# Performance work log

Hardware: AMD Instinct MI355X
Metric: run time of the kernel (lower is better)

Reference implementation:

```python
import jax, jax.numpy as jnp
import numpy as np
from jax.scipy.special import logsumexp

D = 256            # descriptor_dim == output_dim
H = 4              # attention heads (hard-coded in AttentionalGNN)
DH = D // H        # 64 per-head dim
KNN = 20           # k for dynamic kNN graph
N_LAYERS = 18      # ['self','cross'] * 9
SINKHORN_ITERS = 20
MATCH_THRESHOLD = 0.2
BN_EPS = 1e-5
N_KPTS = 1024
B = 1
KENC_CH = [D + 4, D // 4, D // 2, D, 2 * D, D]


def conv1(x, w, b):
    # kernel-size-1 Conv1d: x [B,Cin,N], w [Cout,Cin], b [Cout]
    return jnp.einsum('oc,bcn->bon', w, x) + b[:, None]


def bn(x, g, be):
    # training-mode BatchNorm1d over (batch, length), biased variance
    m = jnp.mean(x, axis=(0, 2), keepdims=True)
    v = jnp.var(x, axis=(0, 2), keepdims=True)
    return g[:, None] * (x - m) * jax.lax.rsqrt(v + BN_EPS) + be[:, None]


def run_kenc(desc, kpts, sc, ws, bs, gs, bes):
    # desc [B,N,D], kpts [B,N,3], sc [B,N] -> [B,D,N]
    x = jnp.concatenate([jnp.swapaxes(desc, 1, 2), jnp.swapaxes(kpts, 1, 2), sc[:, None, :]], axis=1)
    for i in range(4):
        x = jax.nn.relu(bn(conv1(x, ws[i], bs[i]), gs[i], bes[i]))
    return conv1(x, ws[4], bs[4])


def run_chebconv(x, pos, cw, cb):
    # x [1,D,N], pos [1,N,3]; dynamic kNN graph + ChebConv K=3, aggr='add'
    p = pos[0]
    n = p.shape[0]
    g = p @ p.T
    sq = jnp.diagonal(g)
    d = sq[:, None] + sq[None, :] - 2.0 * g           # squared pairwise dist [N,N]
    d = d.at[jnp.arange(n), jnp.arange(n)].set(jnp.inf)  # no self-loops
    _, nbr = jax.lax.top_k(-d, KNN)                   # [N,KNN] neighbor indices
    src = jnp.repeat(jnp.arange(n), KNN)              # query node of each edge
    dst = nbr.reshape(-1)                             # neighbor (message target)
    h = x[0].T                                        # [N,D]
    def prop(t):
        # scaled Laplacian propagation: L_hat edge weight = -1/k (self-loops cancel)
        return jnp.zeros_like(t).at[dst].add(t[src]) * (-1.0 / KNN)
    tx0 = h
    tx1 = prop(tx0)
    tx2 = 2.0 * prop(tx1) - tx0
    out = tx0 @ cw[0].T + tx1 @ cw[1].T + tx2 @ cw[2].T + cb
    return out.T[None]                                # [1,D,N]


def attn_prop(x, src, pw, pb, mw, mb, m1w, m1b, g, be, m2w, m2b):
    # AttentionalPropagation: MHA(x, src, src) then MLP([2D,2D,D]) on concat
    b, _, n = x.shape
    m = src.shape[2]
    q = conv1(x, pw[0], pb[0]).reshape(b, DH, H, n)
    k = conv1(src, pw[1], pb[1]).reshape(b, DH, H, m)
    v = conv1(src, pw[2], pb[2]).reshape(b, DH, H, m)
    scores = jnp.einsum('bdhn,bdhm->bhnm', q, k) / (DH ** 0.5)
    prob = jax.nn.softmax(scores, axis=-1)
    msg = jnp.einsum('bhnm,bdhm->bdhn', prob, v).reshape(b, D, n)
    msg = conv1(msg, mw, mb)
    y = jnp.concatenate([x, msg], axis=1)
    y = jax.nn.relu(bn(conv1(y, m1w, m1b), g, be))
    return conv1(y, m2w, m2b)


def log_optimal_transport(scores, alpha, iters):
    b, m, n = scores.shape
    bins0 = jnp.broadcast_to(alpha, (b, m, 1)).astype(scores.dtype)
    bins1 = jnp.broadcast_to(alpha, (b, 1, n)).astype(scores.dtype)
    binsa = jnp.broadcast_to(alpha, (b, 1, 1)).astype(scores.dtype)
    Z = jnp.concatenate([jnp.concatenate([scores, bins0], 2), jnp.concatenate([bins1, binsa], 2)], 1)
    norm = -np.log(float(m + n))
    log_mu = jnp.concatenate([jnp.full((m,), norm, scores.dtype), jnp.asarray([np.log(float(n)) + norm], scores.dtype)])
    log_nu = jnp.concatenate([jnp.full((n,), norm, scores.dtype), jnp.asarray([np.log(float(m)) + norm], scores.dtype)])
    log_mu = jnp.broadcast_to(log_mu[None], (b, m + 1))
    log_nu = jnp.broadcast_to(log_nu[None], (b, n + 1))
    def step(uv, _):
        u, v = uv
        u = log_mu - logsumexp(Z + v[:, None, :], axis=2)
        v = log_nu - logsumexp(Z + u[:, :, None], axis=1)
        return (u, v), None
    (u, v), _ = jax.lax.scan(step, (jnp.zeros_like(log_mu), jnp.zeros_like(log_nu)), None, length=iters)
    return Z + u[:, :, None] + v[:, None, :] - norm


def _forward(h1, h2, uc1, uc2, sc1, sc2, kws, kbs, kgs, kbes, cheb_w, cheb_b,
             gpw, gpb, gmw, gmb, g1w, g1b, gg, gbe, g2w, g2b, fp_w, fp_b, bin_score):
    d1 = run_kenc(h1, uc1, sc1, kws, kbs, kgs, kbes)
    d2 = run_kenc(h2, uc2, sc2, kws, kbs, kgs, kbes)
    d1 = run_chebconv(d1, uc1, cheb_w, cheb_b)
    d2 = run_chebconv(d2, uc2, cheb_w, cheb_b)
    for i in range(N_LAYERS):
        cross = (i % 2 == 1)
        s0, s1 = (d2, d1) if cross else (d1, d2)
        la = (gpw[i], gpb[i], gmw[i], gmb[i], g1w[i], g1b[i], gg[i], gbe[i], g2w[i], g2b[i])
        delta0 = attn_prop(d1, s0, *la)
        delta1 = attn_prop(d2, s1, *la)
        d1, d2 = d1 + delta0, d2 + delta1
    md1 = conv1(d1, fp_w, fp_b)
    md2 = conv1(d2, fp_w, fp_b)
    sc = jnp.einsum('bdn,bdm->bnm', md1, md2) / (D ** 0.5)
    Z = log_optimal_transport(sc, bin_score, SINKHORN_ITERS)
    return Z, md1, md2


def setup_inputs() -> dict:
    key = jax.random.key(0)
    ks = iter(jax.random.split(key, 64))
    def rn(shape, scale=1.0):
        return jax.random.normal(next(ks), shape, dtype=jnp.float32) * scale
    inp = {}
    inp['h1'] = rn((B, N_KPTS, D))
    inp['h2'] = rn((B, N_KPTS, D))
    for nm in ('unitCartesian1', 'unitCartesian2'):
        p = rn((B, N_KPTS, 3))
        inp[nm] = p / jnp.linalg.norm(p, axis=-1, keepdims=True)
    inp['scores1'] = jax.random.uniform(next(ks), (B, N_KPTS), dtype=jnp.float32)
    inp['scores2'] = jax.random.uniform(next(ks), (B, N_KPTS), dtype=jnp.float32)
    for i in range(5):
        ci, co = KENC_CH[i], KENC_CH[i + 1]
        inp['kenc_w%d' % i] = rn((co, ci), ci ** -0.5)
        inp['kenc_b%d' % i] = jnp.zeros((co,), jnp.float32)
    for i in range(4):
        co = KENC_CH[i + 1]
        inp['kenc_g%d' % i] = jnp.ones((co,), jnp.float32)
        inp['kenc_be%d' % i] = jnp.zeros((co,), jnp.float32)
    inp['cheb_w'] = rn((3, D, D), D ** -0.5)
    inp['cheb_b'] = jnp.zeros((D,), jnp.float32)
    L = N_LAYERS
    inp['gnn_proj_w'] = rn((L, 3, D, D), D ** -0.5)
    inp['gnn_proj_b'] = jnp.zeros((L, 3, D), jnp.float32)
    inp['gnn_merge_w'] = rn((L, D, D), D ** -0.5)
    inp['gnn_merge_b'] = jnp.zeros((L, D), jnp.float32)
    inp['gnn_m1_w'] = rn((L, 2 * D, 2 * D), (2 * D) ** -0.5)
    inp['gnn_m1_b'] = jnp.zeros((L, 2 * D), jnp.float32)
    inp['gnn_g'] = jnp.ones((L, 2 * D), jnp.float32)
    inp['gnn_be'] = jnp.zeros((L, 2 * D), jnp.float32)
    inp['gnn_m2_w'] = rn((L, D, 2 * D), (2 * D) ** -0.5)
    inp['gnn_m2_b'] = jnp.zeros((L, D), jnp.float32)
    inp['fp_w'] = rn((D, D), D ** -0.5)
    inp['fp_b'] = jnp.zeros((D,), jnp.float32)
    inp['bin_score'] = jnp.asarray(1.0, jnp.float32)
    return inp


def reference(h1, h2, unitCartesian1, unitCartesian2, scores1, scores2,
              kenc_w0, kenc_b0, kenc_w1, kenc_b1, kenc_w2, kenc_b2, kenc_w3, kenc_b3, kenc_w4, kenc_b4,
              kenc_g0, kenc_be0, kenc_g1, kenc_be1, kenc_g2, kenc_be2, kenc_g3, kenc_be3,
              cheb_w, cheb_b, gnn_proj_w, gnn_proj_b, gnn_merge_w, gnn_merge_b,
              gnn_m1_w, gnn_m1_b, gnn_g, gnn_be, gnn_m2_w, gnn_m2_b, fp_w, fp_b, bin_score):
    kws = [kenc_w0, kenc_w1, kenc_w2, kenc_w3, kenc_w4]
    kbs = [kenc_b0, kenc_b1, kenc_b2, kenc_b3, kenc_b4]
    kgs = [kenc_g0, kenc_g1, kenc_g2, kenc_g3]
    kbes = [kenc_be0, kenc_be1, kenc_be2, kenc_be3]
    Z, md1, md2 = _forward(h1, h2, unitCartesian1, unitCartesian2, scores1, scores2,
                           kws, kbs, kgs, kbes, cheb_w, cheb_b,
                           gnn_proj_w, gnn_proj_b, gnn_merge_w, gnn_merge_b,
                           gnn_m1_w, gnn_m1_b, gnn_g, gnn_be, gnn_m2_w, gnn_m2_b,
                           fp_w, fp_b, bin_score)
    s = Z[:, :-1, :-1]
    max1v = jnp.max(s, axis=2)
    idx1 = jnp.argmax(s, axis=2)
    idx2 = jnp.argmax(s, axis=1)
    mutual = jnp.arange(s.shape[1])[None, :] == jnp.take_along_axis(idx2, idx1, axis=1)
    mscores = jnp.where(mutual, jnp.exp(max1v), jnp.zeros((), s.dtype))
    valid = mutual & (mscores > MATCH_THRESHOLD)
    matches = jnp.where(valid, idx1, -1).astype(jnp.int32)
    return Z, matches, mscores, md1, md2
```

## Files before the change

### kernel.cpp

```cpp
#include <hip/hip_runtime.h>
#include <math.h>

#define NORM_F  ((float)(-7.6246189861593984953))
#define BIN_F   ((float)(-0.6931471805599453094))

__device__ __forceinline__ float exp_cr(float x) { return (float)exp((double)x); }
__device__ __forceinline__ float log_cr(float x) { return (float)log((double)x); }

struct GJob {
  const float* A0; const float* X0;
  const float* A1; const float* X1;
  const float* A2; const float* X2;
  const float* bias; float* C;
  const float* resid;
};
struct GArgs { GJob j[8]; };

struct TJob { const float* A; const float* B; float* C; int cb; };
struct TArgs { TJob j[8]; };

struct VJob { const float* V; const float* P; float* C; };
struct VArgs { VJob j[8]; };

struct NJob { const float* A; const float* B; float* C; };
struct NArgs { NJob j[2]; };

#define MICRO_FMA(w4, x4)                                   \
  acc[0][0] = fmaf(w4.x, x4.x, acc[0][0]);                  \
  acc[0][1] = fmaf(w4.x, x4.y, acc[0][1]);                  \
  acc[0][2] = fmaf(w4.x, x4.z, acc[0][2]);                  \
  acc[0][3] = fmaf(w4.x, x4.w, acc[0][3]);                  \
  acc[1][0] = fmaf(w4.y, x4.x, acc[1][0]);                  \
  acc[1][1] = fmaf(w4.y, x4.y, acc[1][1]);                  \
  acc[1][2] = fmaf(w4.y, x4.z, acc[1][2]);                  \
  acc[1][3] = fmaf(w4.y, x4.w, acc[1][3]);                  \
  acc[2][0] = fmaf(w4.z, x4.x, acc[2][0]);                  \
  acc[2][1] = fmaf(w4.z, x4.y, acc[2][1]);                  \
  acc[2][2] = fmaf(w4.z, x4.z, acc[2][2]);                  \
  acc[2][3] = fmaf(w4.z, x4.w, acc[2][3]);                  \
  acc[3][0] = fmaf(w4.w, x4.x, acc[3][0]);                  \
  acc[3][1] = fmaf(w4.w, x4.y, acc[3][1]);                  \
  acc[3][2] = fmaf(w4.w, x4.z, acc[3][2]);                  \
  acc[3][3] = fmaf(w4.w, x4.w, acc[3][3]);

__global__ __launch_bounds__(256) void concat_kenc(
    const float* __restrict__ h1, const float* __restrict__ h2,
    const float* __restrict__ uc1, const float* __restrict__ uc2,
    const float* __restrict__ s1, const float* __restrict__ s2,
    float* __restrict__ out) {
  int img = blockIdx.y;
  const float* h  = img ? h2 : h1;
  const float* uc = img ? uc2 : uc1;
  const float* sc = img ? s2 : s1;
  float* o = out + (size_t)img * 260 * 1024;
  int idx = blockIdx.x * 256 + threadIdx.x;
  if (idx >= 260 * 1024) return;
  int c = idx >> 10, n = idx & 1023;
  float v;
  if (c < 256)      v = h[(size_t)n * 256 + c];
  else if (c < 259) v = uc[(size_t)n * 3 + (c - 256)];
  else              v = sc[n];
  o[idx] = v;
}

__global__ __launch_bounds__(256) void gemm_std(GArgs args, int nseg, int split,
                                                int ci0, int ci1, int ci2,
                                                int lda, int co) {
  __shared__ float Wt[32][68];
  __shared__ float Xs[32][68];
  GJob jb = args.j[blockIdx.z];
  const int n0 = blockIdx.x * 64;
  const int c0 = blockIdx.y * 64;
  const int t = threadIdx.x, tx = t & 15, ty = t >> 4;
  float acc[4][4] = {};
  float accT[4][4] = {};
  const float* As[3] = { jb.A0, jb.A1, jb.A2 };
  const float* Xp[3] = { jb.X0, jb.X1, jb.X2 };
  int cis[3] = { ci0, ci1, ci2 };
  for (int s = 0; s < nseg; ++s) {
    const float* A = As[s];
    const float* X = Xp[s];
    const int ci = cis[s];
    if (split) {
      #pragma unroll
      for (int i = 0; i < 4; ++i)
        #pragma unroll
        for (int jj = 0; jj < 4; ++jj) acc[i][jj] = 0.f;
    }
    for (int k0 = 0; k0 < ci; k0 += 32) {
      #pragma unroll
      for (int g = 0; g < 2; ++g) {
        const int row = t >> 2, kk = (t & 3) * 4 + g * 16;
        const float* srcp = A + (size_t)(c0 + row) * lda + k0 + kk;
        float4 w4;
        if (k0 + kk + 4 <= ci) {
          w4 = *(const float4*)srcp;
        } else {
          w4.x = (k0 + kk + 0 < ci) ? srcp[0] : 0.f;
          w4.y = (k0 + kk + 1 < ci) ? srcp[1] : 0.f;
          w4.z = (k0 + kk + 2 < ci) ? srcp[2] : 0.f;
          w4.w = (k0 + kk + 3 < ci) ? srcp[3] : 0.f;
        }
        Wt[kk + 0][row] = w4.x; Wt[kk + 1][row] = w4.y;
        Wt[kk + 2][row] = w4.z; Wt[kk + 3][row] = w4.w;
      }
      #pragma unroll
      for (int g = 0; g < 2; ++g) {
        const int kk = (t >> 4) + g * 16, nl = (t & 15) * 4;
        float4 x4 = make_float4(0.f, 0.f, 0.f, 0.f);
        if (k0 + kk < ci) x4 = *(const float4*)(X + (size_t)(k0 + kk) * 1024 + n0 + nl);
        *(float4*)&Xs[kk][nl] = x4;
      }
      __syncthreads();
      #pragma unroll
      for (int kk = 0; kk < 32; ++kk) {
        const float4 w4 = *(const float4*)&Wt[kk][ty * 4];
        const float4 x4 = *(const float4*)&Xs[kk][tx * 4];
        MICRO_FMA(w4, x4)
      }
      __syncthreads();
    }
    if (split) {
      #pragma unroll
      for (int i = 0; i < 4; ++i)
        #pragma unroll
        for (int jj = 0; jj < 4; ++jj)
          accT[i][jj] = __fadd_rn(accT[i][jj], acc[i][jj]);
    }
  }
  #pragma unroll
  for (int i = 0; i < 4; ++i) {
    const int row = c0 + ty * 4 + i;
    const float b = jb.bias ? jb.bias[row] : 0.f;
    const float* src = split ? accT[i] : acc[i];
    float4 o;
    o.x = __fadd_rn(src[0], b); o.y = __fadd_rn(src[1], b);
    o.z = __fadd_rn(src[2], b); o.w = __fadd_rn(src[3], b);
    if (jb.resid) {
      const float4 r4 = *(const float4*)(jb.resid + (size_t)row * 1024 + n0 + tx * 4);
      o.x = __fadd_rn(r4.x, o.x); o.y = __fadd_rn(r4.y, o.y);
      o.z = __fadd_rn(r4.z, o.z); o.w = __fadd_rn(r4.w, o.w);
    }
    *(float4*)(jb.C + (size_t)row * 1024 + n0 + tx * 4) = o;
  }
}

__global__ __launch_bounds__(256) void gemm_tn(TArgs args, int K, int cs,
                                               float scale, int ldc) {
  __shared__ float As[64][68];
  __shared__ float Bs[64][68];
  TJob jb = args.j[blockIdx.z];
  const int m0 = blockIdx.x * 64;
  const int n0 = blockIdx.y * 64;
  const int t = threadIdx.x, tx = t & 15, ty = t >> 4;
  float acc[4][4] = {};
  for (int k0 = 0; k0 < K; k0 += 64) {
    #pragma unroll
    for (int q = 0; q < 4; ++q) {
      const int kk = (t >> 4) + q * 16;
      const int col = (t & 15) * 4;
      const size_t rb = (size_t)(jb.cb + (k0 + kk) * cs) * 1024;
      *(float4*)&As[kk][col] = *(const float4*)(jb.A + rb + n0 + col);
      *(float4*)&Bs[kk][col] = *(const float4*)(jb.B + rb + m0 + col);
    }
    __syncthreads();
    #pragma unroll 16
    for (int kk = 0; kk < 64; ++kk) {
      const float4 w4 = *(const float4*)&As[kk][ty * 4];
      const float4 x4 = *(const float4*)&Bs[kk][tx * 4];
      MICRO_FMA(w4, x4)
    }
    __syncthreads();
  }
  #pragma unroll
  for (int i = 0; i < 4; ++i) {
    float4 o;
    o.x = __fmul_rn(acc[i][0], scale); o.y = __fmul_rn(acc[i][1], scale);
    o.z = __fmul_rn(acc[i][2], scale); o.w = __fmul_rn(acc[i][3], scale);
    *(float4*)(jb.C + (size_t)(n0 + ty * 4 + i) * ldc + m0 + tx * 4) = o;
  }
}

__global__ __launch_bounds__(256) void gemm_vp(VArgs args) {
  __shared__ float Vs[64][68];
  __shared__ float Ps[64][68];
  VJob jb = args.j[blockIdx.z];
  const int n0 = blockIdx.x * 64;
  const int t = threadIdx.x, tx = t & 15, ty = t >> 4;
  float acc[4][4] = {};
  for (int m0 = 0; m0 < 1024; m0 += 64) {
    const int r = t >> 2;
    #pragma unroll
    for (int q = 0; q < 4; ++q) {
      const int mm = (t & 3) * 4 + q * 16;
      float4 v4 = *(const float4*)(jb.V + (size_t)r * 4096 + m0 + mm);
      Vs[mm + 0][r] = v4.x; Vs[mm + 1][r] = v4.y;
      Vs[mm + 2][r] = v4.z; Vs[mm + 3][r] = v4.w;
      float4 p4 = *(const float4*)(jb.P + (size_t)(n0 + r) * 1024 + m0 + mm);
      Ps[mm + 0][r] = p4.x; Ps[mm + 1][r] = p4.y;
      Ps[mm + 2][r] = p4.z; Ps[mm + 3][r] = p4.w;
    }
    __syncthreads();
    #pragma unroll 16
    for (int mm = 0; mm < 64; ++mm) {
      const float4 w4 = *(const float4*)&Vs[mm][ty * 4];
      const float4 x4 = *(const float4*)&Ps[mm][tx * 4];
      MICRO_FMA(w4, x4)
    }
    __syncthreads();
  }
  #pragma unroll
  for (int i = 0; i < 4; ++i) {
    float4 o;
    o.x = acc[i][0]; o.y = acc[i][1]; o.z = acc[i][2]; o.w = acc[i][3];
    *(float4*)(jb.C + (size_t)(ty * 4 + i) * 4096 + n0 + tx * 4) = o;
  }
}

__global__ __launch_bounds__(256) void gemm_nt(NArgs args, float scale) {
  __shared__ float As[64][68];
  __shared__ float Bs[64][68];
  NJob jb = args.j[blockIdx.z];
  const int d0 = blockIdx.x * 64;
  const int c0 = blockIdx.y * 64;
  const int t = threadIdx.x, tx = t & 15, ty = t >> 4;
  float acc[4][4] = {};
  for (int s0 = 0; s0 < 1024; s0 += 64) {
    const int r = t >> 2;
    #pragma unroll
    for (int q = 0; q < 4; ++q) {
      const int ss = (t & 3) * 4 + q * 16;
      float4 a4 = *(const float4*)(jb.A + (size_t)(c0 + r) * 1024 + s0 + ss);
      As[ss + 0][r] = a4.x; As[ss + 1][r] = a4.y;
      As[ss + 2][r] = a4.z; As[ss + 3][r] = a4.w;
      float4 b4 = *(const float4*)(jb.B + (size_t)(d0 + r) * 1024 + s0 + ss);
      Bs[ss + 0][r] = b4.x; Bs[ss + 1][r] = b4.y;
      Bs[ss + 2][r] = b4.z; Bs[ss + 3][r] = b4.w;
    }
    __syncthreads();
    #pragma unroll 16
    for (int ss = 0; ss < 64; ++ss) {
      const float4 w4 = *(const float4*)&As[ss][ty * 4];
      const float4 x4 = *(const float4*)&Bs[ss][tx * 4];
      MICRO_FMA(w4, x4)
    }
    __syncthreads();
  }
  #pragma unroll
  for (int i = 0; i < 4; ++i) {
    float4 o;
    o.x = __fmul_rn(acc[i][0], scale); o.y = __fmul_rn(acc[i][1], scale);
    o.z = __fmul_rn(acc[i][2], scale); o.w = __fmul_rn(acc[i][3], scale);
    *(float4*)(jb.C + (size_t)(c0 + ty * 4 + i) * 1024 + d0 + tx * 4) = o;
  }
}

__global__ __launch_bounds__(64) void scatter_adj(const int* __restrict__ nbr,
                                                  float* __restrict__ adj) {
  const int i = blockIdx.x, img = blockIdx.y;
  const int t = threadIdx.x;
  if (t >= 20) return;
  const int dst = nbr[((size_t)img * 1024 + i) * 20 + t];
  adj[(size_t)img * 1048576 + (size_t)dst * 1024 + i] = 1.0f;
}

__global__ __launch_bounds__(256) void bn_relu_par(float* __restrict__ x,
                                                   const float* __restrict__ g,
                                                   const float* __restrict__ be,
                                                   int co) {
  const int ch = blockIdx.x, img = blockIdx.y;
  float* p = x + ((size_t)img * co + ch) * 1024;
  __shared__ float ls[1024];
  __shared__ float sh[2];
  const int t = threadIdx.x;
  #pragma unroll
  for (int q = 0; q < 4; ++q) ls[t + q * 256] = p[t + q * 256];
  __syncthreads();
  if (t < 64) {
    float s = 0.f;
    for (int n = 0; n < 1024; ++n) s = __fadd_rn(s, ls[n]);
    const float mean = __fdiv_rn(s, 1024.f);
    float vs = 0.f;
    for (int n = 0; n < 1024; ++n) {
      const float d = __fsub_rn(ls[n], mean);
      vs = __fadd_rn(vs, __fmul_rn(d, d));
    }
    const float var = __fdiv_rn(vs, 1024.f);
    if (t == 0) {
      sh[0] = mean;
      sh[1] = __fdiv_rn(1.f, sqrtf(__fadd_rn(var, 1e-5f)));
    }
  }
  __syncthreads();
  const float mean = sh[0], rs = sh[1];
  const float gc = g[ch], bc = be[ch];
  #pragma unroll
  for (int q = 0; q < 4; ++q) {
    const int n = t + q * 256;
    float v = __fmul_rn(gc, __fsub_rn(ls[n], mean));
    v = __fmul_rn(v, rs);
    v = __fadd_rn(v, bc);
    p[n] = fmaxf(v, 0.f);
  }
}

__global__ __launch_bounds__(256) void knn_kernel(const float* __restrict__ uc1,
                                                  const float* __restrict__ uc2,
                                                  int* __restrict__ nbr) {
  const int i = blockIdx.x, img = blockIdx.y;
  const float* uc = img ? uc2 : uc1;
  __shared__ float dist[1024];
  __shared__ float rv[256];
  __shared__ int   ri[256];
  const int t = threadIdx.x;
  const float pix = uc[i * 3], piy = uc[i * 3 + 1], piz = uc[i * 3 + 2];
  const float sqi = fmaf(piz, piz, fmaf(piy, piy, __fmul_rn(pix, pix)));
  for (int j = t; j < 1024; j += 256) {
    const float x = uc[j * 3], y = uc[j * 3 + 1], z = uc[j * 3 + 2];
    const float gg  = fmaf(piz, z, fmaf(piy, y, __fmul_rn(pix, x)));
    const float sqj = fmaf(z, z, fmaf(y, y, __fmul_rn(x, x)));
    const float d = __fsub_rn(__fadd_rn(sqi, sqj), __fmul_rn(2.f, gg));
    dist[j] = (j == i) ? INFINITY : d;
  }
  __syncthreads();
  int* out = nbr + ((size_t)img * 1024 + i) * 20;
  for (int k = 0; k < 20; ++k) {
    float bv = INFINITY; int bi = 0x7fffffff;
    for (int j = t; j < 1024; j += 256) {
      const float d = dist[j];
      if (d < bv) { bv = d; bi = j; }
    }
    rv[t] = bv; ri[t] = bi;
    __syncthreads();
    for (int st = 128; st > 0; st >>= 1) {
      if (t < st) {
        const float v2 = rv[t + st]; const int i2 = ri[t + st];
        if (v2 < rv[t] || (v2 == rv[t] && i2 < ri[t])) { rv[t] = v2; ri[t] = i2; }
      }
      __syncthreads();
    }
    if (t == 0) { out[k] = ri[0]; dist[ri[0]] = INFINITY; }
    __syncthreads();
  }
}

__global__ __launch_bounds__(256) void axpby(const float* __restrict__ x,
                                             const float* __restrict__ y,
                                             float* __restrict__ o,
                                             float a, float b, int n) {
  const int i = blockIdx.x * 256 + threadIdx.x;
  if (i < n) o[i] = __fadd_rn(__fmul_rn(a, x[i]), __fmul_rn(b, y[i]));
}

__global__ __launch_bounds__(256) void softmax_par(float* __restrict__ P) {
  float* p = P + (size_t)blockIdx.x * 1024;
  __shared__ float ls[1024];
  __shared__ float red[256];
  const int t = threadIdx.x;
  float mx = -INFINITY;
  #pragma unroll
  for (int q = 0; q < 4; ++q) {
    const float v = p[t + q * 256];
    ls[t + q * 256] = v;
    mx = fmaxf(mx, v);
  }
  red[t] = mx;
  __syncthreads();
  for (int st = 128; st > 0; st >>= 1) { if (t < st) red[t] = fmaxf(red[t], red[t + st]); __syncthreads(); }
  mx = red[0];
  __syncthreads();
  #pragma unroll
  for (int q = 0; q < 4; ++q) {
    const int n = t + q * 256;
    ls[n] = exp_cr(__fsub_rn(ls[n], mx));
  }
  __syncthreads();
  if (t < 64) {
    float s = 0.f;
    for (int n = 0; n < 1024; ++n) s = __fadd_rn(s, ls[n]);
    if (t == 0) red[0] = s;
  }
  __syncthreads();
  const float s = red[0];
  #pragma unroll
  for (int q = 0; q < 4; ++q) {
    const int n = t + q * 256;
    p[n] = __fdiv_rn(ls[n], s);
  }
}

__global__ __launch_bounds__(256) void build_Z(const float* __restrict__ sc,
                                               const float* __restrict__ alpha,
                                               float* __restrict__ Z,
                                               float* __restrict__ ZT) {
  const int idx = blockIdx.x * 256 + threadIdx.x;
  if (idx >= 1025 * 1025) return;
  const int i = idx / 1025, j = idx - i * 1025;
  const float v = (i < 1024 && j < 1024) ? sc[(size_t)i * 1024 + j] : alpha[0];
  Z[idx] = v;
  ZT[(size_t)j * 1025 + i] = v;
}

__global__ __launch_bounds__(256) void lse_par(const float* __restrict__ M,
                                               const float* __restrict__ add,
                                               float* __restrict__ out) {
  const int r = blockIdx.x;
  const float* p = M + (size_t)r * 1025;
  __shared__ float ls[1025];
  __shared__ float red[256];
  const int t = threadIdx.x;
  float mx = -INFINITY;
  for (int j = t; j < 1025; j += 256) {
    const float v = __fadd_rn(p[j], add[j]);
    ls[j] = v;
    mx = fmaxf(mx, v);
  }
  red[t] = mx;
  __syncthreads();
  for (int st = 128; st > 0; st >>= 1) { if (t < st) red[t] = fmaxf(red[t], red[t + st]); __syncthreads(); }
  mx = red[0];
  __syncthreads();
  for (int j = t; j < 1025; j += 256) ls[j] = exp_cr(__fsub_rn(ls[j], mx));
  __syncthreads();
  if (t < 64) {
    float s = 0.f;
    for (int j = 0; j < 1025; ++j) s = __fadd_rn(s, ls[j]);
    if (t == 0) {
      const float logw = (r < 1024) ? NORM_F : BIN_F;
      out[r] = __fsub_rn(logw, __fadd_rn(log_cr(s), mx));
    }
  }
}

__global__ __launch_bounds__(256) void write_final(const float* __restrict__ Z,
                                                   const float* __restrict__ u,
                                                   const float* __restrict__ v,
                                                   float* __restrict__ outZ,
                                                   float* __restrict__ FZc) {
  const int idx = blockIdx.x * 256 + threadIdx.x;
  if (idx >= 1025 * 1025) return;
  const int i = idx / 1025, j = idx - i * 1025;
  float t = __fadd_rn(Z[idx], u[i]);
  t = __fadd_rn(t, v[j]);
  t = __fsub_rn(t, NORM_F);
  outZ[idx] = t;
  FZc[(size_t)j * 1025 + i] = t;
}

__global__ __launch_bounds__(256) void argmax_par(const float* __restrict__ M,
                                                  float* __restrict__ maxout,
                                                  int* __restrict__ idxout) {
  const int r = blockIdx.x;
  const float* p = M + (size_t)r * 1025;
  __shared__ float rv[256];
  __shared__ int   ri[256];
  const int t = threadIdx.x;
  float bv = -INFINITY; int bi = 0x7fffffff;
  for (int j = t; j < 1024; j += 256) {
    const float v = p[j];
    if (v > bv) { bv = v; bi = j; }
  }
  rv[t] = bv; ri[t] = bi;
  __syncthreads();
  for (int st = 128; st > 0; st >>= 1) {
    if (t < st) {
      const float v2 = rv[t + st]; const int i2 = ri[t + st];
      if (v2 > rv[t] || (v2 == rv[t] && i2 < ri[t])) { rv[t] = v2; ri[t] = i2; }
    }
    __syncthreads();
  }
  if (t == 0) {
    idxout[r] = ri[0];
    if (maxout) maxout[r] = rv[0];
  }
}

__global__ __launch_bounds__(256) void matches_kernel(const int* __restrict__ idx1,
                                                      const int* __restrict__ idx2,
                                                      const float* __restrict__ rowmax,
                                                      float* __restrict__ m_out,
                                                      float* __restrict__ s_out) {
  const int i = blockIdx.x * 256 + threadIdx.x;
  if (i >= 1024) return;
  const int j = idx1[i];
  const bool mutual = (idx2[j] == i);
  const float msc = mutual ? exp_cr(rowmax[i]) : 0.f;
  s_out[i] = msc;
  m_out[i] = (mutual && msc > 0.2f) ? (float)j : -1.f;
}

extern "C" void kernel_launch(void* const* d_in, const int* in_sizes, int n_in,
                              void* d_out, int out_size, void* d_ws, size_t ws_size,
                              hipStream_t stream) {
  const float* h1  = (const float*)d_in[0];
  const float* h2  = (const float*)d_in[1];
  const float* uc1 = (const float*)d_in[2];
  const float* uc2 = (const float*)d_in[3];
  const float* s1  = (const float*)d_in[4];
  const float* s2  = (const float*)d_in[5];
  const float* kw[5]  = { (const float*)d_in[6],  (const float*)d_in[8],
                          (const float*)d_in[10], (const float*)d_in[12],
                          (const float*)d_in[14] };
  const float* kb[5]  = { (const float*)d_in[7],  (const float*)d_in[9],
                          (const float*)d_in[11], (const float*)d_in[13],
                          (const float*)d_in[15] };
  const float* kg[4]  = { (const float*)d_in[16], (const float*)d_in[18],
                          (const float*)d_in[20], (const float*)d_in[22] };
  const float* kbe[4] = { (const float*)d_in[17], (const float*)d_in[19],
                          (const float*)d_in[21], (const float*)d_in[23] };
  const float* cheb_w = (const float*)d_in[24];
  const float* cheb_b = (const float*)d_in[25];
  const float* pw = (const float*)d_in[26];
  const float* pb = (const float*)d_in[27];
  const float* mw = (const float*)d_in[28];
  const float* mb = (const float*)d_in[29];
  const float* m1w = (const float*)d_in[30];
  const float* m1b = (const float*)d_in[31];
  const float* gg  = (const float*)d_in[32];
  const float* gbe = (const float*)d_in[33];
  const float* m2w = (const float*)d_in[34];
  const float* m2b = (const float*)d_in[35];
  const float* fpw = (const float*)d_in[36];
  const float* fpb = (const float*)d_in[37];
  const float* bin = (const float*)d_in[38];

  float* ws = (float*)d_ws;
  float* A0   = ws;
  float* A1   = ws + 1048576;
  float* Dm   = ws + 2097152;
  float* DT   = ws + 2621440;
  float* TX1  = ws + 3145728;
  float* TX2  = ws + 3670016;
  float* QKV  = ws + 4194304;
  float* PROB = ws + 5767168;
  float* ADJ = PROB;
  float* SCp = PROB;
  float* Zb  = ws;
  float* ZTb = ws + 1050628;
  float* FZc = ws + 3151884;
  float* Ub  = ws + 4202512;
  float* Vb  = ws + 4203540;
  float* RM  = ws + 4204568;
  int*   I1  = (int*)(ws + 4205592);
  int*   I2  = (int*)(ws + 4206616);
  int*   KNNI = (int*)QKV;
  float* MSG   = A1;
  float* DELTA = A1 + 524288;
  float* T1    = A0;
  float* outF  = (float*)d_out;
  float* outZ  = outF;
  float* outM  = outF + 1050625;
  float* outS  = outF + 1051649;
  float* outMD1 = outF + 1052673;
  float* outMD2 = outF + 1314817;
  (void)ws_size; (void)in_sizes; (void)n_in; (void)out_size; (void)DELTA;

  concat_kenc<<<dim3(1040, 2), 256, 0, stream>>>(h1, h2, uc1, uc2, s1, s2, A0);

  const int kci[5] = { 260, 64, 128, 256, 512 };
  const int kco[5] = { 64, 128, 256, 512, 256 };
  float* ping = A0; float* pong = A1;
  for (int L = 0; L < 5; ++L) {
    const int ci = kci[L], co = kco[L];
    float* dst = (L == 4) ? DT : pong;
    GArgs ga = {};
    for (int img = 0; img < 2; ++img) {
      ga.j[img].A0 = kw[L];
      ga.j[img].X0 = ping + (size_t)img * ci * 1024;
      ga.j[img].bias = kb[L];
      ga.j[img].C = dst + (size_t)img * co * 1024;
    }
    gemm_std<<<dim3(16, co / 64, 2), 256, 0, stream>>>(ga, 1, 0, ci, 0, 0, ci, co);
    if (L < 4)
      bn_relu_par<<<dim3(co, 2), 256, 0, stream>>>(dst, kg[L], kbe[L], co);
    float* tmp = ping; ping = pong; pong = tmp;
  }

  knn_kernel<<<dim3(1024, 2), 256, 0, stream>>>(uc1, uc2, KNNI);
  hipMemsetAsync(ADJ, 0, 2u * 1048576u * sizeof(float), stream);
  scatter_adj<<<dim3(1024, 2), 64, 0, stream>>>(KNNI, ADJ);

  {
    NArgs na = {};
    for (int img = 0; img < 2; ++img) {
      na.j[img].A = DT + (size_t)img * 262144;
      na.j[img].B = ADJ + (size_t)img * 1048576;
      na.j[img].C = TX1 + (size_t)img * 262144;
    }
    gemm_nt<<<dim3(16, 4, 2), 256, 0, stream>>>(na, -0.05f);
  }
  {
    NArgs na = {};
    for (int img = 0; img < 2; ++img) {
      na.j[img].A = TX1 + (size_t)img * 262144;
      na.j[img].B = ADJ + (size_t)img * 1048576;
      na.j[img].C = A0 + (size_t)img * 262144;
    }
    gemm_nt<<<dim3(16, 4, 2), 256, 0, stream>>>(na, -0.05f);
  }
  axpby<<<2048, 256, 0, stream>>>(A0, DT, TX2, 2.f, -1.f, 524288);

  {
    GArgs ga = {};
    for (int img = 0; img < 2; ++img) {
      ga.j[img].A0 = cheb_w;           ga.j[img].X0 = DT  + (size_t)img * 262144;
      ga.j[img].A1 = cheb_w + 65536;   ga.j[img].X1 = TX1 + (size_t)img * 262144;
      ga.j[img].A2 = cheb_w + 131072;  ga.j[img].X2 = TX2 + (size_t)img * 262144;
      ga.j[img].bias = cheb_b;
      ga.j[img].C = Dm + (size_t)img * 262144;
    }
    gemm_std<<<dim3(16, 4, 2), 256, 0, stream>>>(ga, 3, 1, 256, 256, 256, 256, 256);
  }

  float* qb = QKV;
  float* kb_ = QKV + 524288;
  float* vb = QKV + 1048576;
  float* MSG2 = QKV;
  for (int l = 0; l < 18; ++l) {
    const int cross = l & 1;
    const float* x[2]   = { Dm, Dm + 262144 };
    const float* src[2] = { cross ? x[1] : x[0], cross ? x[0] : x[1] };

    {
      GArgs ga = {};
      for (int p = 0; p < 3; ++p)
        for (int img = 0; img < 2; ++img) {
          GJob& j = ga.j[p * 2 + img];
          j.A0 = pw + ((size_t)(l * 3 + p)) * 65536;
          j.X0 = (p == 0) ? x[img] : src[img];
          j.bias = pb + ((size_t)(l * 3 + p)) * 256;
          j.C = QKV + ((size_t)(p * 2 + img)) * 262144;
        }
      gemm_std<<<dim3(16, 4, 6), 256, 0, stream>>>(ga, 1, 0, 256, 0, 0, 256, 256);
    }
    {
      TArgs ta = {};
      for (int img = 0; img < 2; ++img)
        for (int h = 0; h < 4; ++h) {
          TJob& j = ta.j[img * 4 + h];
          j.A = qb + (size_t)img * 262144;
          j.B = kb_ + (size_t)img * 262144;
          j.C = PROB + ((size_t)(img * 4 + h)) * 1048576;
          j.cb = h;
        }
      gemm_tn<<<dim3(16, 16, 8), 256, 0, stream>>>(ta, 64, 4, 0.125f, 1024);
    }
    softmax_par<<<8192, 256, 0, stream>>>(PROB);
    {
      VArgs va = {};
      for (int img = 0; img < 2; ++img)
        for (int h = 0; h < 4; ++h) {
          VJob& j = va.j[img * 4 + h];
          j.V = vb + (size_t)img * 262144 + h * 1024;
          j.P = PROB + ((size_t)(img * 4 + h)) * 1048576;
          j.C = MSG + (size_t)img * 262144 + h * 1024;
        }
      gemm_vp<<<dim3(16, 1, 8), 256, 0, stream>>>(va);
    }
    {
      GArgs ga = {};
      for (int img = 0; img < 2; ++img) {
        ga.j[img].A0 = mw + (size_t)l * 65536;
        ga.j[img].X0 = MSG + (size_t)img * 262144;
        ga.j[img].bias = mb + (size_t)l * 256;
        ga.j[img].C = MSG2 + (size_t)img * 262144;
      }
      gemm_std<<<dim3(16, 4, 2), 256, 0, stream>>>(ga, 1, 0, 256, 0, 0, 256, 256);
    }
    {
      GArgs ga = {};
      for (int img = 0; img < 2; ++img) {
        ga.j[img].A0 = m1w + (size_t)l * 262144;        ga.j[img].X0 = x[img];
        ga.j[img].A1 = m1w + (size_t)l * 262144 + 256;  ga.j[img].X1 = MSG2 + (size_t)img * 262144;
        ga.j[img].bias = m1b + (size_t)l * 512;
        ga.j[img].C = T1 + (size_t)img * 524288;
      }
      gemm_std<<<dim3(16, 8, 2), 256, 0, stream>>>(ga, 2, 0, 256, 256, 0, 512, 512);
    }
    bn_relu_par<<<dim3(512, 2), 256, 0, stream>>>(T1, gg + (size_t)l * 512, gbe + (size_t)l * 512, 512);
    {
      GArgs ga = {};
      for (int img = 0; img < 2; ++img) {
        ga.j[img].A0 = m2w + (size_t)l * 131072;
        ga.j[img].X0 = T1 + (size_t)img * 524288;
        ga.j[img].bias = m2b + (size_t)l * 256;
        ga.j[img].C = Dm + (size_t)img * 262144;
        ga.j[img].resid = Dm + (size_t)img * 262144;
      }
      gemm_std<<<dim3(16, 4, 2), 256, 0, stream>>>(ga, 1, 0, 512, 0, 0, 512, 256);
    }
  }

  {
    GArgs ga = {};
    for (int img = 0; img < 2; ++img) {
      ga.j[img].A0 = fpw;
      ga.j[img].X0 = Dm + (size_t)img * 262144;
      ga.j[img].bias = fpb;
      ga.j[img].C = (img ? outMD2 : outMD1);
    }
    gemm_std<<<dim3(16, 4, 2), 256, 0, stream>>>(ga, 1, 0, 256, 0, 0, 256, 256);
  }
  {
    TArgs ta = {};
    ta.j[0].A = outMD1; ta.j[0].B = outMD2; ta.j[0].C = SCp; ta.j[0].cb = 0;
    gemm_tn<<<dim3(16, 16, 1), 256, 0, stream>>>(ta, 256, 1, 0.0625f, 1024);
  }

  build_Z<<<4105, 256, 0, stream>>>(SCp, bin, Zb, ZTb);
  hipMemsetAsync(Ub, 0, 1025 * sizeof(float), stream);
  hipMemsetAsync(Vb, 0, 1025 * sizeof(float), stream);
  for (int it = 0; it < 20; ++it) {
    lse_par<<<1025, 256, 0, stream>>>(Zb, Vb, Ub);
    lse_par<<<1025, 256, 0, stream>>>(ZTb, Ub, Vb);
  }
  write_final<<<4105, 256, 0, stream>>>(Zb, Ub, Vb, outZ, FZc);

  argmax_par<<<1024, 256, 0, stream>>>(outZ, RM, I1);
  argmax_par<<<1024, 256, 0, stream>>>(FZc, (float*)nullptr, I2);
  matches_kernel<<<4, 256, 0, stream>>>(I1, I2, RM, outM, outS);
}
```

Before: 5.385 ms.

## Retile GEMM kernels with 8x8 register microtiles and rebalanced grids

The conv-style GEMM now runs as a templated 64-thread kernel where each thread computes an 8x8 output block, and the split-accumulation flag becomes a compile-time parameter. The attention score GEMM moves to 128x128 tiles with 8x8 per-thread accumulators. The V·P and adjacency GEMMs are split along the output-channel dimension into 32-row slices with 128-thread blocks to launch more blocks. The goal is higher arithmetic intensity per shared-memory load in the score GEMM and better occupancy in the skinny GEMMs. The risks are fewer blocks for the 64x64 GEMMs (only 64 threads each) and higher register pressure from the 128 accumulators per thread.

```diff
diff --git a/kernel.cpp b/kernel.cpp
--- a/kernel.cpp
+++ b/kernel.cpp
@@ -63,17 +63,18 @@
   o[idx] = v;
 }
 
-__global__ __launch_bounds__(256) void gemm_std(GArgs args, int nseg, int split,
-                                                int ci0, int ci1, int ci2,
-                                                int lda, int co) {
+template<int SPLIT>
+__global__ __launch_bounds__(64) void gemm_std_t(GArgs args, int nseg,
+                                                 int ci0, int ci1, int ci2,
+                                                 int lda, int co) {
   __shared__ float Wt[32][68];
   __shared__ float Xs[32][68];
   GJob jb = args.j[blockIdx.z];
   const int n0 = blockIdx.x * 64;
   const int c0 = blockIdx.y * 64;
-  const int t = threadIdx.x, tx = t & 15, ty = t >> 4;
-  float acc[4][4] = {};
-  float accT[4][4] = {};
+  const int t = threadIdx.x, tx = t & 7, ty = t >> 3;
+  float acc[8][8] = {};
+  float accT[8][8] = {};
   const float* As[3] = { jb.A0, jb.A1, jb.A2 };
   const float* Xp[3] = { jb.X0, jb.X1, jb.X2 };
   int cis[3] = { ci0, ci1, ci2 };
@@ -81,32 +82,35 @@
     const float* A = As[s];
     const float* X = Xp[s];
     const int ci = cis[s];
-    if (split) {
+    if (SPLIT) {
       #pragma unroll
-      for (int i = 0; i < 4; ++i)
+      for (int i = 0; i < 8; ++i)
         #pragma unroll
-        for (int jj = 0; jj < 4; ++jj) acc[i][jj] = 0.f;
+        for (int jj = 0; jj < 8; ++jj) acc[i][jj] = 0.f;
     }
     for (int k0 = 0; k0 < ci; k0 += 32) {
-      #pragma unroll
-      for (int g = 0; g < 2; ++g) {
-        const int row = t >> 2, kk = (t & 3) * 4 + g * 16;
-        const float* srcp = A + (size_t)(c0 + row) * lda + k0 + kk;
-        float4 w4;
-        if (k0 + kk + 4 <= ci) {
-          w4 = *(const float4*)srcp;
-        } else {
-          w4.x = (k0 + kk + 0 < ci) ? srcp[0] : 0.f;
-          w4.y = (k0 + kk + 1 < ci) ? srcp[1] : 0.f;
-          w4.z = (k0 + kk + 2 < ci) ? srcp[2] : 0.f;
-          w4.w = (k0 + kk + 3 < ci) ? srcp[3] : 0.f;
+      {
+        const float* srcp = A + (size_t)(c0 + t) * lda + k0;
+        #pragma unroll
+        for (int g = 0; g < 8; ++g) {
+          const int kk = g * 4;
+          float4 w4;
+          if (k0 + kk + 4 <= ci) {
+            w4 = *(const float4*)(srcp + kk);
+          } else {
+            w4.x = (k0 + kk + 0 < ci) ? srcp[kk + 0] : 0.f;
+            w4.y = (k0 + kk + 1 < ci) ? srcp[kk + 1] : 0.f;
+            w4.z = (k0 + kk + 2 < ci) ? srcp[kk + 2] : 0.f;
+            w4.w = (k0 + kk + 3 < ci) ? srcp[kk + 3] : 0.f;
+          }
+          Wt[kk + 0][t] = w4.x; Wt[kk + 1][t] = w4.y;
+          Wt[kk + 2][t] = w4.z; Wt[kk + 3][t] = w4.w;
         }
-        Wt[kk + 0][row] = w4.x; Wt[kk + 1][row] = w4.y;
-        Wt[kk + 2][row] = w4.z; Wt[kk + 3][row] = w4.w;
       }
       #pragma unroll
-      for (int g = 0; g < 2; ++g) {
-        const int kk = (t >> 4) + g * 16, nl = (t & 15) * 4;
+      for (int g = 0; g < 8; ++g) {
+        const int kk = (t >> 4) + g * 4;
+        const int nl = (t & 15) * 4;
         float4 x4 = make_float4(0.f, 0.f, 0.f, 0.f);
         if (k0 + kk < ci) x4 = *(const float4*)(X + (size_t)(k0 + kk) * 1024 + n0 + nl);
         *(float4*)&Xs[kk][nl] = x4;
@@ -114,94 +118,123 @@
       __syncthreads();
       #pragma unroll
       for (int kk = 0; kk < 32; ++kk) {
-        const float4 w4 = *(const float4*)&Wt[kk][ty * 4];
-        const float4 x4 = *(const float4*)&Xs[kk][tx * 4];
-        MICRO_FMA(w4, x4)
+        float w[8], xv[8];
+        *(float4*)&w[0]  = *(const float4*)&Wt[kk][ty * 8];
+        *(float4*)&w[4]  = *(const float4*)&Wt[kk][ty * 8 + 4];
+        *(float4*)&xv[0] = *(const float4*)&Xs[kk][tx * 8];
+        *(float4*)&xv[4] = *(const float4*)&Xs[kk][tx * 8 + 4];
+        #pragma unroll
+        for (int i = 0; i < 8; ++i)
+          #pragma unroll
+          for (int jj = 0; jj < 8; ++jj)
+            acc[i][jj] = fmaf(w[i], xv[jj], acc[i][jj]);
       }
       __syncthreads();
     }
-    if (split) {
+    if (SPLIT) {
       #pragma unroll
-      for (int i = 0; i < 4; ++i)
+      for (int i = 0; i < 8; ++i)
         #pragma unroll
-        for (int jj = 0; jj < 4; ++jj)
+        for (int jj = 0; jj < 8; ++jj)
           accT[i][jj] = __fadd_rn(accT[i][jj], acc[i][jj]);
     }
   }
   #pragma unroll
-  for (int i = 0; i < 4; ++i) {
-    const int row = c0 + ty * 4 + i;
+  for (int i = 0; i < 8; ++i) {
+    const int row = c0 + ty * 8 + i;
     const float b = jb.bias ? jb.bias[row] : 0.f;
-    const float* src = split ? accT[i] : acc[i];
-    float4 o;
-    o.x = __fadd_rn(src[0], b); o.y = __fadd_rn(src[1], b);
-    o.z = __fadd_rn(src[2], b); o.w = __fadd_rn(src[3], b);
-    if (jb.resid) {
-      const float4 r4 = *(const float4*)(jb.resid + (size_t)row * 1024 + n0 + tx * 4);
-      o.x = __fadd_rn(r4.x, o.x); o.y = __fadd_rn(r4.y, o.y);
-      o.z = __fadd_rn(r4.z, o.z); o.w = __fadd_rn(r4.w, o.w);
-    }
-    *(float4*)(jb.C + (size_t)row * 1024 + n0 + tx * 4) = o;
+    const float* src = SPLIT ? accT[i] : acc[i];
+    #pragma unroll
+    for (int hh = 0; hh < 2; ++hh) {
+      float4 o;
+      o.x = __fadd_rn(src[hh * 4 + 0], b); o.y = __fadd_rn(src[hh * 4 + 1], b);
+      o.z = __fadd_rn(src[hh * 4 + 2], b); o.w = __fadd_rn(src[hh * 4 + 3], b);
+      if (jb.resid) {
+        const float4 r4 = *(const float4*)(jb.resid + (size_t)row * 1024 + n0 + tx * 8 + hh * 4);
+        o.x = __fadd_rn(r4.x, o.x); o.y = __fadd_rn(r4.y, o.y);
+        o.z = __fadd_rn(r4.z, o.z); o.w = __fadd_rn(r4.w, o.w);
+      }
+      *(float4*)(jb.C + (size_t)row * 1024 + n0 + tx * 8 + hh * 4) = o;
+    }
   }
 }
 
 __global__ __launch_bounds__(256) void gemm_tn(TArgs args, int K, int cs,
                                                float scale, int ldc) {
-  __shared__ float As[64][68];
-  __shared__ float Bs[64][68];
+  __shared__ float As[32][132];
+  __shared__ float Bs[32][132];
   TJob jb = args.j[blockIdx.z];
-  const int m0 = blockIdx.x * 64;
-  const int n0 = blockIdx.y * 64;
+  const int m0 = blockIdx.x * 128;
+  const int n0 = blockIdx.y * 128;
   const int t = threadIdx.x, tx = t & 15, ty = t >> 4;
-  float acc[4][4] = {};
-  for (int k0 = 0; k0 < K; k0 += 64) {
+  float acc[8][8] = {};
+  for (int k0 = 0; k0 < K; k0 += 32) {
     #pragma unroll
     for (int q = 0; q < 4; ++q) {
-      const int kk = (t >> 4) + q * 16;
-      const int col = (t & 15) * 4;
+      const int idx = t + q * 256;
+      const int kk = idx >> 5;
+      const int c4 = (idx & 31) * 4;
       const size_t rb = (size_t)(jb.cb + (k0 + kk) * cs) * 1024;
-      *(float4*)&As[kk][col] = *(const float4*)(jb.A + rb + n0 + col);
-      *(float4*)&Bs[kk][col] = *(const float4*)(jb.B + rb + m0 + col);
-    }
-    __syncthreads();
-    #pragma unroll 16
-    for (int kk = 0; kk < 64; ++kk) {
-      const float4 w4 = *(const float4*)&As[kk][ty * 4];
-      const float4 x4 = *(const float4*)&Bs[kk][tx * 4];
-      MICRO_FMA(w4, x4)
-    }
-    __syncthreads();
-  }
-  #pragma unroll
-  for (int i = 0; i < 4; ++i) {
-    float4 o;
-    o.x = __fmul_rn(acc[i][0], scale); o.y = __fmul_rn(acc[i][1], scale);
-    o.z = __fmul_rn(acc[i][2], scale); o.w = __fmul_rn(acc[i][3], scale);
-    *(float4*)(jb.C + (size_t)(n0 + ty * 4 + i) * ldc + m0 + tx * 4) = o;
-  }
-}
-
-__global__ __launch_bounds__(256) void gemm_vp(VArgs args) {
-  __shared__ float Vs[64][68];
+      *(float4*)&As[kk][c4] = *(const float4*)(jb.A + rb + n0 + c4);
+      *(float4*)&Bs[kk][c4] = *(const float4*)(jb.B + rb + m0 + c4);
+    }
+    __syncthreads();
+    #pragma unroll
+    for (int kk = 0; kk < 32; ++kk) {
+      float w[8], xv[8];
+      *(float4*)&w[0]  = *(const float4*)&As[kk][ty * 8];
+      *(float4*)&w[4]  = *(const float4*)&As[kk][ty * 8 + 4];
+      *(float4*)&xv[0] = *(const float4*)&Bs[kk][tx * 8];
+      *(float4*)&xv[4] = *(const float4*)&Bs[kk][tx * 8 + 4];
+      #pragma unroll
+      for (int i = 0; i < 8; ++i)
+        #pragma unroll
+        for (int jj = 0; jj < 8; ++jj)
+          acc[i][jj] = fmaf(w[i], xv[jj], acc[i][jj]);
+    }
+    __syncthreads();
+  }
+  #pragma unroll
+  for (int i = 0; i < 8; ++i) {
+    #pragma unroll
+    for (int hh = 0; hh < 2; ++hh) {
+      float4 o;
+      o.x = __fmul_rn(acc[i][hh * 4 + 0], scale);
+      o.y = __fmul_rn(acc[i][hh * 4 + 1], scale);
+      o.z = __fmul_rn(acc[i][hh * 4 + 2], scale);
+      o.w = __fmul_rn(acc[i][hh * 4 + 3], scale);
+      *(float4*)(jb.C + (size_t)(n0 + ty * 8 + i) * ldc + m0 + tx * 8 + hh * 4) = o;
+    }
+  }
+}
+
+__global__ __launch_bounds__(128) void gemm_vp(VArgs args) {
+  __shared__ float Vs[64][36];
   __shared__ float Ps[64][68];
   VJob jb = args.j[blockIdx.z];
   const int n0 = blockIdx.x * 64;
+  const int d0 = blockIdx.y * 32;
   const int t = threadIdx.x, tx = t & 15, ty = t >> 4;
   float acc[4][4] = {};
   for (int m0 = 0; m0 < 1024; m0 += 64) {
-    const int r = t >> 2;
     #pragma unroll
     for (int q = 0; q < 4; ++q) {
-      const int mm = (t & 3) * 4 + q * 16;
-      float4 v4 = *(const float4*)(jb.V + (size_t)r * 4096 + m0 + mm);
-      Vs[mm + 0][r] = v4.x; Vs[mm + 1][r] = v4.y;
-      Vs[mm + 2][r] = v4.z; Vs[mm + 3][r] = v4.w;
-      float4 p4 = *(const float4*)(jb.P + (size_t)(n0 + r) * 1024 + m0 + mm);
-      Ps[mm + 0][r] = p4.x; Ps[mm + 1][r] = p4.y;
-      Ps[mm + 2][r] = p4.z; Ps[mm + 3][r] = p4.w;
-    }
-    __syncthreads();
-    #pragma unroll 16
+      const int idx = t + q * 128;
+      const int d = idx >> 4, m4 = (idx & 15) * 4;
+      float4 v4 = *(const float4*)(jb.V + (size_t)(d0 + d) * 4096 + m0 + m4);
+      Vs[m4 + 0][d] = v4.x; Vs[m4 + 1][d] = v4.y;
+      Vs[m4 + 2][d] = v4.z; Vs[m4 + 3][d] = v4.w;
+    }
+    #pragma unroll
+    for (int q = 0; q < 8; ++q) {
+      const int idx = t + q * 128;
+      const int n = idx >> 4, m4 = (idx & 15) * 4;
+      float4 p4 = *(const float4*)(jb.P + (size_t)(n0 + n) * 1024 + m0 + m4);
+      Ps[m4 + 0][n] = p4.x; Ps[m4 + 1][n] = p4.y;
+      Ps[m4 + 2][n] = p4.z; Ps[m4 + 3][n] = p4.w;
+    }
+    __syncthreads();
+    #pragma unroll
     for (int mm = 0; mm < 64; ++mm) {
       const float4 w4 = *(const float4*)&Vs[mm][ty * 4];
       const float4 x4 = *(const float4*)&Ps[mm][tx * 4];
@@ -213,35 +246,40 @@
   for (int i = 0; i < 4; ++i) {
     float4 o;
     o.x = acc[i][0]; o.y = acc[i][1]; o.z = acc[i][2]; o.w = acc[i][3];
-    *(float4*)(jb.C + (size_t)(ty * 4 + i) * 4096 + n0 + tx * 4) = o;
-  }
-}
-
-__global__ __launch_bounds__(256) void gemm_nt(NArgs args, float scale) {
-  __shared__ float As[64][68];
-  __shared__ float Bs[64][68];
+    *(float4*)(jb.C + (size_t)(d0 + ty * 4 + i) * 4096 + n0 + tx * 4) = o;
+  }
+}
+
+__global__ __launch_bounds__(128) void gemm_nt(NArgs args, float scale) {
+  __shared__ float Cs[64][36];
+  __shared__ float Ds[64][68];
   NJob jb = args.j[blockIdx.z];
   const int d0 = blockIdx.x * 64;
-  const int c0 = blockIdx.y * 64;
+  const int c0 = blockIdx.y * 32;
   const int t = threadIdx.x, tx = t & 15, ty = t >> 4;
   float acc[4][4] = {};
   for (int s0 = 0; s0 < 1024; s0 += 64) {
-    const int r = t >> 2;
     #pragma unroll
     for (int q = 0; q < 4; ++q) {
-      const int ss = (t & 3) * 4 + q * 16;
-      float4 a4 = *(const float4*)(jb.A + (size_t)(c0 + r) * 1024 + s0 + ss);
-      As[ss + 0][r] = a4.x; As[ss + 1][r] = a4.y;
-      As[ss + 2][r] = a4.z; As[ss + 3][r] = a4.w;
-      float4 b4 = *(const float4*)(jb.B + (size_t)(d0 + r) * 1024 + s0 + ss);
-      Bs[ss + 0][r] = b4.x; Bs[ss + 1][r] = b4.y;
-      Bs[ss + 2][r] = b4.z; Bs[ss + 3][r] = b4.w;
-    }
-    __syncthreads();
-    #pragma unroll 16
+      const int idx = t + q * 128;
+      const int c = idx >> 4, s4 = (idx & 15) * 4;
+      float4 a4 = *(const float4*)(jb.A + (size_t)(c0 + c) * 1024 + s0 + s4);
+      Cs[s4 + 0][c] = a4.x; Cs[s4 + 1][c] = a4.y;
+      Cs[s4 + 2][c] = a4.z; Cs[s4 + 3][c] = a4.w;
+    }
+    #pragma unroll
+    for (int q = 0; q < 8; ++q) {
+      const int idx = t + q * 128;
+      const int d = idx >> 4, s4 = (idx & 15) * 4;
+      float4 b4 = *(const float4*)(jb.B + (size_t)(d0 + d) * 1024 + s0 + s4);
+      Ds[s4 + 0][d] = b4.x; Ds[s4 + 1][d] = b4.y;
+      Ds[s4 + 2][d] = b4.z; Ds[s4 + 3][d] = b4.w;
+    }
+    __syncthreads();
+    #pragma unroll
     for (int ss = 0; ss < 64; ++ss) {
-      const float4 w4 = *(const float4*)&As[ss][ty * 4];
-      const float4 x4 = *(const float4*)&Bs[ss][tx * 4];
+      const float4 w4 = *(const float4*)&Cs[ss][ty * 4];
+      const float4 x4 = *(const float4*)&Ds[ss][tx * 4];
       MICRO_FMA(w4, x4)
     }
     __syncthreads();
@@ -545,7 +583,6 @@
   int*   I2  = (int*)(ws + 4206616);
   int*   KNNI = (int*)QKV;
   float* MSG   = A1;
-  float* DELTA = A1 + 524288;
   float* T1    = A0;
   float* outF  = (float*)d_out;
   float* outZ  = outF;
@@ -553,7 +590,7 @@
   float* outS  = outF + 1051649;
   float* outMD1 = outF + 1052673;
   float* outMD2 = outF + 1314817;
-  (void)ws_size; (void)in_sizes; (void)n_in; (void)out_size; (void)DELTA;
+  (void)ws_size; (void)in_sizes; (void)n_in; (void)out_size;
 
   concat_kenc<<<dim3(1040, 2), 256, 0, stream>>>(h1, h2, uc1, uc2, s1, s2, A0);
 
@@ -570,7 +607,7 @@
       ga.j[img].bias = kb[L];
       ga.j[img].C = dst + (size_t)img * co * 1024;
     }
-    gemm_std<<<dim3(16, co / 64, 2), 256, 0, stream>>>(ga, 1, 0, ci, 0, 0, ci, co);
+    gemm_std_t<0><<<dim3(16, co / 64, 2), 64, 0, stream>>>(ga, 1, ci, 0, 0, ci, co);
     if (L < 4)
       bn_relu_par<<<dim3(co, 2), 256, 0, stream>>>(dst, kg[L], kbe[L], co);
     float* tmp = ping; ping = pong; pong = tmp;
@@ -587,7 +624,7 @@
       na.j[img].B = ADJ + (size_t)img * 1048576;
       na.j[img].C = TX1 + (size_t)img * 262144;
     }
-    gemm_nt<<<dim3(16, 4, 2), 256, 0, stream>>>(na, -0.05f);
+    gemm_nt<<<dim3(16, 8, 2), 128, 0, stream>>>(na, -0.05f);
   }
   {
     NArgs na = {};
@@ -596,7 +633,7 @@
       na.j[img].B = ADJ + (size_t)img * 1048576;
       na.j[img].C = A0 + (size_t)img * 262144;
     }
-    gemm_nt<<<dim3(16, 4, 2), 256, 0, stream>>>(na, -0.05f);
+    gemm_nt<<<dim3(16, 8, 2), 128, 0, stream>>>(na, -0.05f);
   }
   axpby<<<2048, 256, 0, stream>>>(A0, DT, TX2, 2.f, -1.f, 524288);
 
@@ -609,7 +646,7 @@
       ga.j[img].bias = cheb_b;
       ga.j[img].C = Dm + (size_t)img * 262144;
     }
-    gemm_std<<<dim3(16, 4, 2), 256, 0, stream>>>(ga, 3, 1, 256, 256, 256, 256, 256);
+    gemm_std_t<1><<<dim3(16, 4, 2), 64, 0, stream>>>(ga, 3, 256, 256, 256, 256, 256);
   }
 
   float* qb = QKV;
@@ -631,7 +668,7 @@
           j.bias = pb + ((size_t)(l * 3 + p)) * 256;
           j.C = QKV + ((size_t)(p * 2 + img)) * 262144;
         }
-      gemm_std<<<dim3(16, 4, 6), 256, 0, stream>>>(ga, 1, 0, 256, 0, 0, 256, 256);
+      gemm_std_t<0><<<dim3(16, 4, 6), 64, 0, stream>>>(ga, 1, 256, 0, 0, 256, 256);
     }
     {
       TArgs ta = {};
@@ -643,7 +680,7 @@
           j.C = PROB + ((size_t)(img * 4 + h)) * 1048576;
           j.cb = h;
         }
-      gemm_tn<<<dim3(16, 16, 8), 256, 0, stream>>>(ta, 64, 4, 0.125f, 1024);
+      gemm_tn<<<dim3(8, 8, 8), 256, 0, stream>>>(ta, 64, 4, 0.125f, 1024);
     }
     softmax_par<<<8192, 256, 0, stream>>>(PROB);
     {
@@ -655,7 +692,7 @@
           j.P = PROB + ((size_t)(img * 4 + h)) * 1048576;
           j.C = MSG + (size_t)img * 262144 + h * 1024;
         }
-      gemm_vp<<<dim3(16, 1, 8), 256, 0, stream>>>(va);
+      gemm_vp<<<dim3(16, 2, 8), 128, 0, stream>>>(va);
     }
     {
       GArgs ga = {};
@@ -665,7 +702,7 @@
         ga.j[img].bias = mb + (size_t)l * 256;
         ga.j[img].C = MSG2 + (size_t)img * 262144;
       }
-      gemm_std<<<dim3(16, 4, 2), 256, 0, stream>>>(ga, 1, 0, 256, 0, 0, 256, 256);
+      gemm_std_t<0><<<dim3(16, 4, 2), 64, 0, stream>>>(ga, 1, 256, 0, 0, 256, 256);
     }
     {
       GArgs ga = {};
@@ -675,7 +712,7 @@
         ga.j[img].bias = m1b + (size_t)l * 512;
         ga.j[img].C = T1 + (size_t)img * 524288;
       }
-      gemm_std<<<dim3(16, 8, 2), 256, 0, stream>>>(ga, 2, 0, 256, 256, 0, 512, 512);
+      gemm_std_t<0><<<dim3(16, 8, 2), 64, 0, stream>>>(ga, 2, 256, 256, 0, 512, 512);
     }
     bn_relu_par<<<dim3(512, 2), 256, 0, stream>>>(T1, gg + (size_t)l * 512, gbe + (size_t)l * 512, 512);
     {
@@ -687,7 +724,7 @@
         ga.j[img].C = Dm + (size_t)img * 262144;
         ga.j[img].resid = Dm + (size_t)img * 262144;
       }
-      gemm_std<<<dim3(16, 4, 2), 256, 0, stream>>>(ga, 1, 0, 512, 0, 0, 512, 256);
+      gemm_std_t<0><<<dim3(16, 4, 2), 64, 0, stream>>>(ga, 1, 512, 0, 0, 512, 256);
     }
   }
 
@@ -699,12 +736,12 @@
       ga.j[img].bias = fpb;
       ga.j[img].C = (img ? outMD2 : outMD1);
     }
-    gemm_std<<<dim3(16, 4, 2), 256, 0, stream>>>(ga, 1, 0, 256, 0, 0, 256, 256);
+    gemm_std_t<0><<<dim3(16, 4, 2), 64, 0, stream>>>(ga, 1, 256, 0, 0, 256, 256);
   }
   {
     TArgs ta = {};
     ta.j[0].A = outMD1; ta.j[0].B = outMD2; ta.j[0].C = SCp; ta.j[0].cb = 0;
-    gemm_tn<<<dim3(16, 16, 1), 256, 0, stream>>>(ta, 256, 1, 0.0625f, 1024);
+    gemm_tn<<<dim3(8, 8, 1), 256, 0, stream>>>(ta, 256, 1, 0.0625f, 1024);
   }
 
   build_Z<<<4105, 256, 0, stream>>>(SCp, bin, Zb, ZTb);
```

New measurement: 8.583 ms. 1.59x slower.
